# Kernel optimization log

Hardware: AMD Instinct MI355X
Metric: run time of the kernel (lower is better)

## Reference

```python
import jax, jax.numpy as jnp
import numpy as np

B, C, D, K = 16, 512, 256, 32

def setup_inputs() -> dict:
    key = jax.random.key(0)
    ks = jax.random.split(key, 6)
    s = 1.0 / np.sqrt(D)
    return {
        "h": jax.random.normal(ks[0], (B, C, D), dtype=jnp.float32),
        "topk_idx": jax.random.randint(ks[1], (B, C, K), 0, C, dtype=jnp.int64),
        "topk_scores": jax.random.normal(ks[2], (B, C, K), dtype=jnp.float32),
        "vW": jax.random.normal(ks[3], (D, D), dtype=jnp.float32) * s,
        "vb": jnp.zeros((D,), dtype=jnp.float32),
        "oW": jax.random.normal(ks[4], (D, D), dtype=jnp.float32) * s,
        "ob": jnp.zeros((D,), dtype=jnp.float32),
        "gW": jax.random.normal(ks[5], (2 * D, D), dtype=jnp.float32) * s,
        "gb": jnp.zeros((D,), dtype=jnp.float32),
    }

def reference(h, topk_idx, topk_scores, vW, vb, oW, ob, gW, gb):
    # Gather K neighbor features per (batch, channel): [B, C, K, D]
    b_idx = jnp.arange(h.shape[0])[:, None, None]
    neigh = h[b_idx, topk_idx]                         # [B,C,K,D]
    attn = jax.nn.softmax(topk_scores, axis=-1)        # [B,C,K]
    neigh = jnp.einsum('bckd,de->bcke', neigh, vW) + vb  # v_proj
    agg = jnp.einsum('bck,bckd->bcd', attn, neigh)      # weighted sum
    gate = jax.nn.sigmoid(jnp.concatenate([h, agg], axis=-1) @ gW + gb)
    delta = gate * (agg @ oW + ob)
    return delta
```

## Files before the change

### kernel.cpp

```cpp
#include <hip/hip_runtime.h>
#include <hip/hip_bf16.h>
#include <cstdint>
#include <cstddef>

using short8  = __attribute__((ext_vector_type(8))) short;
using short4v = __attribute__((ext_vector_type(4))) short;
using f32x4   = __attribute__((ext_vector_type(4))) float;

constexpr int NB = 16, NC = 512, ND = 256, NK = 32;
constexpr int ROWS = 16;
constexpr int NROW = NB * NC;
constexpr int NBLK = NROW / ROWS;
constexpr int LDP  = ND + 8;
constexpr int PLD  = 516;

constexpr int LDS_W   = 16 * PLD * 4;
constexpr int LDS_HB  = LDS_W + 16 * LDP * 2;
constexpr int LDS_TOT = LDS_HB + 16 * LDP * 2;

constexpr int PVW = 0;
constexpr int POW = 65536;
constexpr int PGW = 131072;
constexpr int PHB = 262144;
constexpr size_t WS_NEED = (size_t)(PHB + NB * 131072) * 2;

static __device__ __forceinline__ unsigned short f2bf(float f) {
    __hip_bfloat16 b = __float2bfloat16(f);
    return *reinterpret_cast<unsigned short*>(&b);
}
static __device__ __forceinline__ short4v f2bf4(float4 v) {
    short4v r;
    r[0] = (short)f2bf(v.x); r[1] = (short)f2bf(v.y);
    r[2] = (short)f2bf(v.z); r[3] = (short)f2bf(v.w);
    return r;
}

__global__ __launch_bounds__(256)
void stk_pack_all(const float* __restrict__ vW, const float* __restrict__ oW,
                  const float* __restrict__ gW, const float* __restrict__ h,
                  unsigned short* __restrict__ ws)
{
    const int blk = blockIdx.x;
    if (blk < 128) {
        const int tid  = blk * 256 + threadIdx.x;
        const int lane = tid & 63;
        const int fl   = tid >> 6;
        const float* src; int nt, ks;
        if (fl < 128)      { src = vW; nt = fl >> 3;         ks = fl & 7;          }
        else if (fl < 256) { src = oW; nt = (fl - 128) >> 3; ks = (fl - 128) & 7;  }
        else               { src = gW; nt = (fl - 256) >> 4; ks = (fl - 256) & 15; }
        const int col = nt * 16 + (lane & 15);
        const int k0  = ks * 32 + (lane >> 4) * 8;
        short8 v;
        #pragma unroll
        for (int j = 0; j < 8; ++j)
            v[j] = (short)f2bf(src[(size_t)(k0 + j) * ND + col]);
        *reinterpret_cast<short8*>(&ws[(size_t)tid * 8]) = v;
    } else {
        const int tid  = (blk - 128) * 256 + threadIdx.x;
        const int lane = tid & 63;
        const int fs   = tid >> 6;
        const int b    = fs >> 8;
        const int ks   = (fs >> 4) & 15;
        const int nt   = fs & 15;
        const float* src = h + (size_t)b * NC * ND;
        const int col = nt * 16 + (lane & 15);
        const int k0  = ks * 32 + (lane >> 4) * 8;
        short8 v;
        #pragma unroll
        for (int j = 0; j < 8; ++j)
            v[j] = (short)f2bf(src[(size_t)(k0 + j) * ND + col]);
        *reinterpret_cast<short8*>(&ws[(size_t)PHB + (size_t)tid * 8]) = v;
    }
}

__global__ __launch_bounds__(512, 4)
void stk_mfma(const float* __restrict__ h,
              const int*   __restrict__ topk_idx,
              const float* __restrict__ topk_scores,
              const float* __restrict__ vb, const float* __restrict__ ob,
              const float* __restrict__ gb,
              const unsigned short* __restrict__ wsb,
              float* __restrict__ out)
{
    __shared__ __align__(16) char smem[LDS_TOT];
    float          (*s_P )[PLD] = reinterpret_cast<float(*)[PLD]>(smem);
    unsigned short (*s_ab)[LDP] = reinterpret_cast<unsigned short(*)[LDP]>(smem);
    unsigned short (*s_w )[LDP] = reinterpret_cast<unsigned short(*)[LDP]>(smem + LDS_W);
    unsigned short (*s_hb)[LDP] = reinterpret_cast<unsigned short(*)[LDP]>(smem + LDS_HB);

    const int t     = threadIdx.x;
    const int bid   = (int)blockIdx.x;
    const int swz   = ((bid & 7) << 6) + (bid >> 3);
    const int m0    = swz * ROWS;
    const int batch = m0 >> 9;

    {
        float4* p4 = reinterpret_cast<float4*>(&s_P[0][0]);
        #pragma unroll
        for (int i = 0; i < 5; ++i) {
            const int j = t + i * 512;
            if (j < (ROWS * PLD) / 4) p4[j] = float4{0.f, 0.f, 0.f, 0.f};
        }
    }

    const int sr  = t >> 5;
    const int sc8 = (t & 31) * 8;
    const float4 h0 = *reinterpret_cast<const float4*>(&h[(size_t)(m0 + sr) * ND + sc8]);
    const float4 h1 = *reinterpret_cast<const float4*>(&h[(size_t)(m0 + sr) * ND + sc8 + 4]);

    const int k = t & 31;
    const int r = t >> 5;
    float att; int id;
    {
        const size_t off = (size_t)(m0 + r) * NK + k;
        const float s = topk_scores[off];
        id = topk_idx[off];
        float m = s;
        #pragma unroll
        for (int msk = 16; msk >= 1; msk >>= 1)
            m = fmaxf(m, __shfl_xor(m, msk));
        const float p = __expf(s - m);
        float Z = p;
        #pragma unroll
        for (int msk = 16; msk >= 1; msk >>= 1)
            Z += __shfl_xor(Z, msk);
        att = p / Z;
    }
    __syncthreads();

    atomicAdd(&s_P[r][id], att);

    *reinterpret_cast<short4v*>(&s_hb[sr][sc8])     = f2bf4(h0);
    *reinterpret_cast<short4v*>(&s_hb[sr][sc8 + 4]) = f2bf4(h1);
    __syncthreads();

    const int lane = t & 63;
    const int w    = t >> 6;
    const int n0   = 2 * w;
    const int lr   = lane & 15;
    const int lg   = lane >> 4;

    {
        f32x4 acc[2] = {f32x4{0,0,0,0}, f32x4{0,0,0,0}};
        const unsigned short* hf = wsb + (size_t)PHB + (size_t)batch * 131072;
        #pragma unroll
        for (int ks = 0; ks < 16; ++ks) {
            const int kb = ks * 32 + lg * 8;
            const float4 a0 = *reinterpret_cast<const float4*>(&s_P[lr][kb]);
            const float4 a1 = *reinterpret_cast<const float4*>(&s_P[lr][kb + 4]);
            short8 a;
            a[0] = (short)f2bf(a0.x); a[1] = (short)f2bf(a0.y);
            a[2] = (short)f2bf(a0.z); a[3] = (short)f2bf(a0.w);
            a[4] = (short)f2bf(a1.x); a[5] = (short)f2bf(a1.y);
            a[6] = (short)f2bf(a1.z); a[7] = (short)f2bf(a1.w);
            #pragma unroll
            for (int n = 0; n < 2; ++n) {
                const short8 b = *reinterpret_cast<const short8*>(
                    &hf[(size_t)(((ks * 16 + n0 + n) * 64 + lane) * 8)]);
                acc[n] = __builtin_amdgcn_mfma_f32_16x16x32_bf16(a, b, acc[n], 0, 0, 0);
            }
        }
        #pragma unroll
        for (int n = 0; n < 2; ++n) {
            const int col = (n0 + n) * 16 + lr;
            #pragma unroll
            for (int q = 0; q < 4; ++q)
                s_w[4 * lg + q][col] = f2bf(acc[n][q]);
        }
    }
    __syncthreads();

    {
        f32x4 acc[2];
        #pragma unroll
        for (int n = 0; n < 2; ++n) {
            const float bv = vb[(n0 + n) * 16 + lr];
            acc[n] = f32x4{bv, bv, bv, bv};
        }
        #pragma unroll
        for (int ks = 0; ks < 8; ++ks) {
            const int kb = ks * 32 + lg * 8;
            const short8 a = *reinterpret_cast<const short8*>(&s_w[lr][kb]);
            #pragma unroll
            for (int n = 0; n < 2; ++n) {
                const short8 b = *reinterpret_cast<const short8*>(
                    &wsb[(size_t)(PVW + (((n0 + n) * 8 + ks) * 64 + lane) * 8)]);
                acc[n] = __builtin_amdgcn_mfma_f32_16x16x32_bf16(a, b, acc[n], 0, 0, 0);
            }
        }
        #pragma unroll
        for (int n = 0; n < 2; ++n) {
            const int col = (n0 + n) * 16 + lr;
            #pragma unroll
            for (int q = 0; q < 4; ++q)
                s_ab[4 * lg + q][col] = f2bf(acc[n][q]);
        }
    }
    __syncthreads();

    {
        f32x4 ao[2], ag[2];
        #pragma unroll
        for (int n = 0; n < 2; ++n) {
            const float bo = ob[(n0 + n) * 16 + lr];
            const float bg = gb[(n0 + n) * 16 + lr];
            ao[n] = f32x4{bo, bo, bo, bo};
            ag[n] = f32x4{bg, bg, bg, bg};
        }
        #pragma unroll
        for (int ks = 0; ks < 8; ++ks) {
            const int kb = ks * 32 + lg * 8;
            const short8 aa = *reinterpret_cast<const short8*>(&s_ab[lr][kb]);
            const short8 ah = *reinterpret_cast<const short8*>(&s_hb[lr][kb]);
            #pragma unroll
            for (int n = 0; n < 2; ++n) {
                const int nt = n0 + n;
                const short8 b_o  = *reinterpret_cast<const short8*>(
                    &wsb[(size_t)(POW + ((nt * 8 + ks) * 64 + lane) * 8)]);
                const short8 b_g1 = *reinterpret_cast<const short8*>(
                    &wsb[(size_t)(PGW + ((nt * 16 + ks) * 64 + lane) * 8)]);
                const short8 b_g2 = *reinterpret_cast<const short8*>(
                    &wsb[(size_t)(PGW + ((nt * 16 + ks + 8) * 64 + lane) * 8)]);
                ao[n] = __builtin_amdgcn_mfma_f32_16x16x32_bf16(aa, b_o,  ao[n], 0, 0, 0);
                ag[n] = __builtin_amdgcn_mfma_f32_16x16x32_bf16(ah, b_g1, ag[n], 0, 0, 0);
                ag[n] = __builtin_amdgcn_mfma_f32_16x16x32_bf16(aa, b_g2, ag[n], 0, 0, 0);
            }
        }
        #pragma unroll
        for (int n = 0; n < 2; ++n) {
            const int col = (n0 + n) * 16 + lr;
            #pragma unroll
            for (int q = 0; q < 4; ++q) {
                const int row = m0 + 4 * lg + q;
                const float g = 1.f / (1.f + __expf(-ag[n][q]));
                out[(size_t)row * ND + col] = g * ao[n][q];
            }
        }
    }
}

__global__ __launch_bounds__(512, 2)
void stk_fused(const float* __restrict__ h,
               const int*   __restrict__ topk_idx,
               const float* __restrict__ topk_scores,
               const float* __restrict__ vW, const float* __restrict__ vb,
               const float* __restrict__ oW, const float* __restrict__ ob,
               const float* __restrict__ gW, const float* __restrict__ gb,
               float* __restrict__ out)
{
    __shared__ float s_attn[32][NK];
    __shared__ int   s_idx [32][NK];
    __shared__ float s_wsum[32][ND];
    __shared__ float s_h   [32][ND];
    __shared__ float s_agg [32][ND];

    const int t  = threadIdx.x;
    const int m0 = blockIdx.x * 32;
    const size_t hb = (size_t)(m0 >> 9) * NC * ND;

    {
        const int k  = t & 31;
        const int r0 = t >> 5;
        #pragma unroll
        for (int half = 0; half < 2; ++half) {
            const int r = r0 + (half << 4);
            const size_t off = (size_t)(m0 + r) * NK + k;
            const float s = topk_scores[off];
            const int  id = topk_idx[off];
            float m = s;
            #pragma unroll
            for (int msk = 16; msk >= 1; msk >>= 1) m = fmaxf(m, __shfl_xor(m, msk));
            const float p = __expf(s - m);
            float Z = p;
            #pragma unroll
            for (int msk = 16; msk >= 1; msk >>= 1) Z += __shfl_xor(Z, msk);
            s_attn[r][k] = p / Z;
            s_idx [r][k] = id;
        }
    }
    __syncthreads();

    const int d  = t & 127;
    const int rb = (t >> 7) * 8;

    #pragma unroll
    for (int i = 0; i < 8; ++i) {
        const int r = rb + i;
        const size_t ro = (size_t)(m0 + r) * ND;
        s_h[r][d]       = h[ro + d];
        s_h[r][d + 128] = h[ro + d + 128];
    }
    #pragma unroll 1
    for (int i = 0; i < 8; ++i) {
        const int r = rb + i;
        float a0 = 0.f, a1 = 0.f;
        #pragma unroll 8
        for (int k = 0; k < NK; ++k) {
            const float w  = s_attn[r][k];
            const size_t nb = hb + (size_t)s_idx[r][k] * ND;
            a0 = fmaf(w, h[nb + d],       a0);
            a1 = fmaf(w, h[nb + d + 128], a1);
        }
        s_wsum[r][d]       = a0;
        s_wsum[r][d + 128] = a1;
    }
    __syncthreads();

    float agg0[8], agg1[8];
    {
        const float b0 = vb[d], b1 = vb[d + 128];
        #pragma unroll
        for (int i = 0; i < 8; ++i) { agg0[i] = b0; agg1[i] = b1; }
        for (int e0 = 0; e0 < ND; e0 += 4) {
            float w0[4], w1[4];
            #pragma unroll
            for (int j = 0; j < 4; ++j) {
                w0[j] = vW[(size_t)(e0 + j) * ND + d];
                w1[j] = vW[(size_t)(e0 + j) * ND + d + 128];
            }
            #pragma unroll
            for (int i = 0; i < 8; ++i) {
                const float4 a = *reinterpret_cast<const float4*>(&s_wsum[rb + i][e0]);
                agg0[i] = fmaf(a.x, w0[0], agg0[i]); agg1[i] = fmaf(a.x, w1[0], agg1[i]);
                agg0[i] = fmaf(a.y, w0[1], agg0[i]); agg1[i] = fmaf(a.y, w1[1], agg1[i]);
                agg0[i] = fmaf(a.z, w0[2], agg0[i]); agg1[i] = fmaf(a.z, w1[2], agg1[i]);
                agg0[i] = fmaf(a.w, w0[3], agg0[i]); agg1[i] = fmaf(a.w, w1[3], agg1[i]);
            }
        }
        #pragma unroll
        for (int i = 0; i < 8; ++i) {
            s_agg[rb + i][d]       = agg0[i];
            s_agg[rb + i][d + 128] = agg1[i];
        }
    }
    __syncthreads();

    float o0[8], o1[8], g0[8], g1[8];
    {
        const float obb0 = ob[d], obb1 = ob[d + 128];
        const float gbb0 = gb[d], gbb1 = gb[d + 128];
        #pragma unroll
        for (int i = 0; i < 8; ++i) { o0[i]=obb0; o1[i]=obb1; g0[i]=gbb0; g1[i]=gbb1; }
        for (int e0 = 0; e0 < ND; e0 += 4) {
            float ow0[4], ow1[4], gh0[4], gh1[4], ga0[4], ga1[4];
            #pragma unroll
            for (int j = 0; j < 4; ++j) {
                const size_t er = (size_t)(e0 + j) * ND;
                ow0[j] = oW[er + d];                    ow1[j] = oW[er + d + 128];
                gh0[j] = gW[er + d];                    gh1[j] = gW[er + d + 128];
                ga0[j] = gW[er + (size_t)ND * ND + d];  ga1[j] = gW[er + (size_t)ND * ND + d + 128];
            }
            #pragma unroll
            for (int i = 0; i < 8; ++i) {
                const float4 a  = *reinterpret_cast<const float4*>(&s_agg[rb + i][e0]);
                const float4 hh = *reinterpret_cast<const float4*>(&s_h  [rb + i][e0]);
                o0[i] = fmaf(a.x, ow0[0], o0[i]); o0[i] = fmaf(a.y, ow0[1], o0[i]);
                o0[i] = fmaf(a.z, ow0[2], o0[i]); o0[i] = fmaf(a.w, ow0[3], o0[i]);
                o1[i] = fmaf(a.x, ow1[0], o1[i]); o1[i] = fmaf(a.y, ow1[1], o1[i]);
                o1[i] = fmaf(a.z, ow1[2], o1[i]); o1[i] = fmaf(a.w, ow1[3], o1[i]);
                g0[i] = fmaf(hh.x, gh0[0], g0[i]); g0[i] = fmaf(hh.y, gh0[1], g0[i]);
                g0[i] = fmaf(hh.z, gh0[2], g0[i]); g0[i] = fmaf(hh.w, gh0[3], g0[i]);
                g1[i] = fmaf(hh.x, gh1[0], g1[i]); g1[i] = fmaf(hh.y, gh1[1], g1[i]);
                g1[i] = fmaf(hh.z, gh1[2], g1[i]); g1[i] = fmaf(hh.w, gh1[3], g1[i]);
                g0[i] = fmaf(a.x, ga0[0], g0[i]); g0[i] = fmaf(a.y, ga0[1], g0[i]);
                g0[i] = fmaf(a.z, ga0[2], g0[i]); g0[i] = fmaf(a.w, ga0[3], g0[i]);
                g1[i] = fmaf(a.x, ga1[0], g1[i]); g1[i] = fmaf(a.y, ga1[1], g1[i]);
                g1[i] = fmaf(a.z, ga1[2], g1[i]); g1[i] = fmaf(a.w, ga1[3], g1[i]);
            }
        }
    }
    #pragma unroll
    for (int i = 0; i < 8; ++i) {
        const size_t ro = (size_t)(m0 + rb + i) * ND;
        const float sg0 = 1.f / (1.f + __expf(-g0[i]));
        const float sg1 = 1.f / (1.f + __expf(-g1[i]));
        out[ro + d]       = sg0 * o0[i];
        out[ro + d + 128] = sg1 * o1[i];
    }
}

extern "C" void kernel_launch(void* const* d_in, const int* in_sizes, int n_in,
                              void* d_out, int out_size, void* d_ws, size_t ws_size,
                              hipStream_t stream) {
    const float* h   = (const float*)d_in[0];
    const int*   idx = (const int*)  d_in[1];
    const float* sc  = (const float*)d_in[2];
    const float* vW  = (const float*)d_in[3];
    const float* vb  = (const float*)d_in[4];
    const float* oW  = (const float*)d_in[5];
    const float* ob  = (const float*)d_in[6];
    const float* gW  = (const float*)d_in[7];
    const float* gb  = (const float*)d_in[8];
    float* out = (float*)d_out;

    if (ws_size >= WS_NEED) {
        unsigned short* wsb = (unsigned short*)d_ws;
        stk_pack_all<<<1152, 256, 0, stream>>>(vW, oW, gW, h, wsb);
        stk_mfma    <<<NBLK, 512, 0, stream>>>(h, idx, sc, vb, ob, gb, wsb, out);
    } else {
        stk_fused<<<256, 512, 0, stream>>>(h, idx, sc, vW, vb, oW, ob, gW, gb, out);
    }
}
```

Measured before the change: 31.85 us.

## Double rows per block and reuse each weight fragment across two M tiles

Each block now handles 32 rows with 1024 threads (16 waves), and each wave owns one 16-column N tile while looping over two 16-row M tiles. Each B fragment loaded from global memory (packed h, vW, oW, gW) is reused for two MFMAs, which halves weight traffic per row. The cost is half as many blocks (256), larger LDS per block and launch bounds of 1024 with one block per CU, which lowers occupancy and latency hiding. The per-thread softmax and atomic setup remains one thread per (row, k).

```diff
diff --git a/kernel.cpp b/kernel.cpp
--- a/kernel.cpp
+++ b/kernel.cpp
@@ -8,15 +8,16 @@
 using f32x4   = __attribute__((ext_vector_type(4))) float;
 
 constexpr int NB = 16, NC = 512, ND = 256, NK = 32;
-constexpr int ROWS = 16;
+constexpr int ROWS = 32;
 constexpr int NROW = NB * NC;
 constexpr int NBLK = NROW / ROWS;
+constexpr int NTHR = 1024;
 constexpr int LDP  = ND + 8;
 constexpr int PLD  = 516;
 
-constexpr int LDS_W   = 16 * PLD * 4;
-constexpr int LDS_HB  = LDS_W + 16 * LDP * 2;
-constexpr int LDS_TOT = LDS_HB + 16 * LDP * 2;
+constexpr int LDS_W   = ROWS * PLD * 4;
+constexpr int LDS_HB  = LDS_W + ROWS * LDP * 2;
+constexpr int LDS_TOT = LDS_HB + ROWS * LDP * 2;
 
 constexpr int PVW = 0;
 constexpr int POW = 65536;
@@ -74,7 +75,7 @@
     }
 }
 
-__global__ __launch_bounds__(512, 4)
+__global__ __launch_bounds__(1024, 1)
 void stk_mfma(const float* __restrict__ h,
               const int*   __restrict__ topk_idx,
               const float* __restrict__ topk_scores,
@@ -89,17 +90,17 @@
     unsigned short (*s_w )[LDP] = reinterpret_cast<unsigned short(*)[LDP]>(smem + LDS_W);
     unsigned short (*s_hb)[LDP] = reinterpret_cast<unsigned short(*)[LDP]>(smem + LDS_HB);
 
-    const int t     = threadIdx.x;
-    const int bid   = (int)blockIdx.x;
-    const int swz   = ((bid & 7) << 6) + (bid >> 3);
-    const int m0    = swz * ROWS;
+    const int t   = threadIdx.x;
+    const int bid = (int)blockIdx.x;
+    const int swz = ((bid & 7) << 5) + (bid >> 3);
+    const int m0  = swz * ROWS;
     const int batch = m0 >> 9;
 
     {
         float4* p4 = reinterpret_cast<float4*>(&s_P[0][0]);
         #pragma unroll
         for (int i = 0; i < 5; ++i) {
-            const int j = t + i * 512;
+            const int j = t + i * NTHR;
             if (j < (ROWS * PLD) / 4) p4[j] = float4{0.f, 0.f, 0.f, 0.f};
         }
     }
@@ -137,7 +138,7 @@
 
     const int lane = t & 63;
     const int w    = t >> 6;
-    const int n0   = 2 * w;
+    const int nt   = w;
     const int lr   = lane & 15;
     const int lg   = lane >> 4;
 
@@ -147,94 +148,85 @@
         #pragma unroll
         for (int ks = 0; ks < 16; ++ks) {
             const int kb = ks * 32 + lg * 8;
-            const float4 a0 = *reinterpret_cast<const float4*>(&s_P[lr][kb]);
-            const float4 a1 = *reinterpret_cast<const float4*>(&s_P[lr][kb + 4]);
-            short8 a;
-            a[0] = (short)f2bf(a0.x); a[1] = (short)f2bf(a0.y);
-            a[2] = (short)f2bf(a0.z); a[3] = (short)f2bf(a0.w);
-            a[4] = (short)f2bf(a1.x); a[5] = (short)f2bf(a1.y);
-            a[6] = (short)f2bf(a1.z); a[7] = (short)f2bf(a1.w);
-            #pragma unroll
-            for (int n = 0; n < 2; ++n) {
-                const short8 b = *reinterpret_cast<const short8*>(
-                    &hf[(size_t)(((ks * 16 + n0 + n) * 64 + lane) * 8)]);
-                acc[n] = __builtin_amdgcn_mfma_f32_16x16x32_bf16(a, b, acc[n], 0, 0, 0);
-            }
-        }
-        #pragma unroll
-        for (int n = 0; n < 2; ++n) {
-            const int col = (n0 + n) * 16 + lr;
+            const short8 b = *reinterpret_cast<const short8*>(
+                &hf[(size_t)(((ks * 16 + nt) * 64 + lane) * 8)]);
+            #pragma unroll
+            for (int m = 0; m < 2; ++m) {
+                const float4 a0 = *reinterpret_cast<const float4*>(&s_P[m * 16 + lr][kb]);
+                const float4 a1 = *reinterpret_cast<const float4*>(&s_P[m * 16 + lr][kb + 4]);
+                short8 a;
+                a[0] = (short)f2bf(a0.x); a[1] = (short)f2bf(a0.y);
+                a[2] = (short)f2bf(a0.z); a[3] = (short)f2bf(a0.w);
+                a[4] = (short)f2bf(a1.x); a[5] = (short)f2bf(a1.y);
+                a[6] = (short)f2bf(a1.z); a[7] = (short)f2bf(a1.w);
+                acc[m] = __builtin_amdgcn_mfma_f32_16x16x32_bf16(a, b, acc[m], 0, 0, 0);
+            }
+        }
+        #pragma unroll
+        for (int m = 0; m < 2; ++m) {
+            const int col = nt * 16 + lr;
             #pragma unroll
             for (int q = 0; q < 4; ++q)
-                s_w[4 * lg + q][col] = f2bf(acc[n][q]);
-        }
-    }
-    __syncthreads();
-
-    {
-        f32x4 acc[2];
-        #pragma unroll
-        for (int n = 0; n < 2; ++n) {
-            const float bv = vb[(n0 + n) * 16 + lr];
-            acc[n] = f32x4{bv, bv, bv, bv};
-        }
+                s_w[m * 16 + 4 * lg + q][col] = f2bf(acc[m][q]);
+        }
+    }
+    __syncthreads();
+
+    {
+        const float bv = vb[nt * 16 + lr];
+        f32x4 acc[2] = {f32x4{bv, bv, bv, bv}, f32x4{bv, bv, bv, bv}};
         #pragma unroll
         for (int ks = 0; ks < 8; ++ks) {
             const int kb = ks * 32 + lg * 8;
-            const short8 a = *reinterpret_cast<const short8*>(&s_w[lr][kb]);
-            #pragma unroll
-            for (int n = 0; n < 2; ++n) {
-                const short8 b = *reinterpret_cast<const short8*>(
-                    &wsb[(size_t)(PVW + (((n0 + n) * 8 + ks) * 64 + lane) * 8)]);
-                acc[n] = __builtin_amdgcn_mfma_f32_16x16x32_bf16(a, b, acc[n], 0, 0, 0);
-            }
-        }
-        #pragma unroll
-        for (int n = 0; n < 2; ++n) {
-            const int col = (n0 + n) * 16 + lr;
+            const short8 b = *reinterpret_cast<const short8*>(
+                &wsb[(size_t)(PVW + ((nt * 8 + ks) * 64 + lane) * 8)]);
+            #pragma unroll
+            for (int m = 0; m < 2; ++m) {
+                const short8 a = *reinterpret_cast<const short8*>(&s_w[m * 16 + lr][kb]);
+                acc[m] = __builtin_amdgcn_mfma_f32_16x16x32_bf16(a, b, acc[m], 0, 0, 0);
+            }
+        }
+        #pragma unroll
+        for (int m = 0; m < 2; ++m) {
+            const int col = nt * 16 + lr;
             #pragma unroll
             for (int q = 0; q < 4; ++q)
-                s_ab[4 * lg + q][col] = f2bf(acc[n][q]);
-        }
-    }
-    __syncthreads();
-
-    {
-        f32x4 ao[2], ag[2];
-        #pragma unroll
-        for (int n = 0; n < 2; ++n) {
-            const float bo = ob[(n0 + n) * 16 + lr];
-            const float bg = gb[(n0 + n) * 16 + lr];
-            ao[n] = f32x4{bo, bo, bo, bo};
-            ag[n] = f32x4{bg, bg, bg, bg};
-        }
+                s_ab[m * 16 + 4 * lg + q][col] = f2bf(acc[m][q]);
+        }
+    }
+    __syncthreads();
+
+    {
+        const float bo = ob[nt * 16 + lr];
+        const float bg = gb[nt * 16 + lr];
+        f32x4 ao[2] = {f32x4{bo, bo, bo, bo}, f32x4{bo, bo, bo, bo}};
+        f32x4 ag[2] = {f32x4{bg, bg, bg, bg}, f32x4{bg, bg, bg, bg}};
         #pragma unroll
         for (int ks = 0; ks < 8; ++ks) {
             const int kb = ks * 32 + lg * 8;
-            const short8 aa = *reinterpret_cast<const short8*>(&s_ab[lr][kb]);
-            const short8 ah = *reinterpret_cast<const short8*>(&s_hb[lr][kb]);
-            #pragma unroll
-            for (int n = 0; n < 2; ++n) {
-                const int nt = n0 + n;
-                const short8 b_o  = *reinterpret_cast<const short8*>(
-                    &wsb[(size_t)(POW + ((nt * 8 + ks) * 64 + lane) * 8)]);
-                const short8 b_g1 = *reinterpret_cast<const short8*>(
-                    &wsb[(size_t)(PGW + ((nt * 16 + ks) * 64 + lane) * 8)]);
-                const short8 b_g2 = *reinterpret_cast<const short8*>(
-                    &wsb[(size_t)(PGW + ((nt * 16 + ks + 8) * 64 + lane) * 8)]);
-                ao[n] = __builtin_amdgcn_mfma_f32_16x16x32_bf16(aa, b_o,  ao[n], 0, 0, 0);
-                ag[n] = __builtin_amdgcn_mfma_f32_16x16x32_bf16(ah, b_g1, ag[n], 0, 0, 0);
-                ag[n] = __builtin_amdgcn_mfma_f32_16x16x32_bf16(aa, b_g2, ag[n], 0, 0, 0);
-            }
-        }
-        #pragma unroll
-        for (int n = 0; n < 2; ++n) {
-            const int col = (n0 + n) * 16 + lr;
+            const short8 b_o  = *reinterpret_cast<const short8*>(
+                &wsb[(size_t)(POW + ((nt * 8 + ks) * 64 + lane) * 8)]);
+            const short8 b_g1 = *reinterpret_cast<const short8*>(
+                &wsb[(size_t)(PGW + ((nt * 16 + ks) * 64 + lane) * 8)]);
+            const short8 b_g2 = *reinterpret_cast<const short8*>(
+                &wsb[(size_t)(PGW + ((nt * 16 + ks + 8) * 64 + lane) * 8)]);
+            #pragma unroll
+            for (int m = 0; m < 2; ++m) {
+                const short8 aa = *reinterpret_cast<const short8*>(&s_ab[m * 16 + lr][kb]);
+                const short8 ah = *reinterpret_cast<const short8*>(&s_hb[m * 16 + lr][kb]);
+                ao[m] = __builtin_amdgcn_mfma_f32_16x16x32_bf16(aa, b_o,  ao[m], 0, 0, 0);
+                ag[m] = __builtin_amdgcn_mfma_f32_16x16x32_bf16(ah, b_g1, ag[m], 0, 0, 0);
+                ag[m] = __builtin_amdgcn_mfma_f32_16x16x32_bf16(aa, b_g2, ag[m], 0, 0, 0);
+            }
+        }
+        #pragma unroll
+        for (int m = 0; m < 2; ++m) {
+            const int col = nt * 16 + lr;
             #pragma unroll
             for (int q = 0; q < 4; ++q) {
-                const int row = m0 + 4 * lg + q;
-                const float g = 1.f / (1.f + __expf(-ag[n][q]));
-                out[(size_t)row * ND + col] = g * ao[n][q];
+                const int row = m0 + m * 16 + 4 * lg + q;
+                const float g = 1.f / (1.f + __expf(-ag[m][q]));
+                out[(size_t)row * ND + col] = g * ao[m][q];
             }
         }
     }
@@ -397,7 +389,7 @@
     if (ws_size >= WS_NEED) {
         unsigned short* wsb = (unsigned short*)d_ws;
         stk_pack_all<<<1152, 256, 0, stream>>>(vW, oW, gW, h, wsb);
-        stk_mfma    <<<NBLK, 512, 0, stream>>>(h, idx, sc, vb, ob, gb, wsb, out);
+        stk_mfma    <<<NBLK, NTHR, 0, stream>>>(h, idx, sc, vb, ob, gb, wsb, out);
     } else {
         stk_fused<<<256, 512, 0, stream>>>(h, idx, sc, vW, vb, oW, ob, gW, gb, out);
     }
```

New measurement: 33.41 us. 1.05x slower.

## Precompute h·vW and h·gW_h per batch; aggregate projected features, double rows per block

Applied to the files above, without the earlier changes.

Uses linearity: the value projection is applied to h once per row in a prep kernel (HV = h·vW + vb), so agg becomes P·HV directly, removing the per-block vW GEMM. The h half of the gate GEMM is also precomputed in prep and stored as bf16 accumulator fragments, which are loaded to initialise the gate accumulators. The main kernel now handles 32 rows per block and reuses each B fragment across two M tiles. This moves more work into the prep kernel, which reads unpacked fp32 weights directly, and adds extra bf16 rounding of the intermediate results.

```diff
diff --git a/kernel.cpp b/kernel.cpp
--- a/kernel.cpp
+++ b/kernel.cpp
@@ -8,25 +8,26 @@
 using f32x4   = __attribute__((ext_vector_type(4))) float;
 
 constexpr int NB = 16, NC = 512, ND = 256, NK = 32;
-constexpr int ROWS = 16;
+constexpr int ROWS = 32;
 constexpr int NROW = NB * NC;
 constexpr int NBLK = NROW / ROWS;
 constexpr int LDP  = ND + 8;
 constexpr int PLD  = 516;
 
-constexpr int LDS_W   = 16 * PLD * 4;
-constexpr int LDS_HB  = LDS_W + 16 * LDP * 2;
-constexpr int LDS_TOT = LDS_HB + 16 * LDP * 2;
-
-constexpr int PVW = 0;
-constexpr int POW = 65536;
-constexpr int PGW = 131072;
-constexpr int PHB = 262144;
-constexpr size_t WS_NEED = (size_t)(PHB + NB * 131072) * 2;
+constexpr int LDS_TOT = ROWS * PLD * 4;
+
+constexpr int POW2 = 0;
+constexpr int PGA  = 65536;
+constexpr int PGH  = 131072;
+constexpr int PHV  = 131072 + 2097152;
+constexpr size_t WS_NEED = (size_t)(PHV + NB * 131072) * 2;
 
 static __device__ __forceinline__ unsigned short f2bf(float f) {
     __hip_bfloat16 b = __float2bfloat16(f);
     return *reinterpret_cast<unsigned short*>(&b);
+}
+static __device__ __forceinline__ float bf2f(unsigned short u) {
+    return __uint_as_float(((unsigned)u) << 16);
 }
 static __device__ __forceinline__ short4v f2bf4(float4 v) {
     short4v r;
@@ -35,87 +36,152 @@
     return r;
 }
 
-__global__ __launch_bounds__(256)
-void stk_pack_all(const float* __restrict__ vW, const float* __restrict__ oW,
-                  const float* __restrict__ gW, const float* __restrict__ h,
-                  unsigned short* __restrict__ ws)
+__global__ __launch_bounds__(512)
+void stk_prep(const float* __restrict__ vW, const float* __restrict__ vb,
+              const float* __restrict__ oW,
+              const float* __restrict__ gW, const float* __restrict__ gb,
+              const float* __restrict__ h, unsigned short* __restrict__ ws)
 {
+    __shared__ __align__(16) unsigned short s_a[32][264];
+    __shared__ __align__(16) unsigned short s_c[32][264];
     const int blk = blockIdx.x;
-    if (blk < 128) {
-        const int tid  = blk * 256 + threadIdx.x;
+    const int t   = threadIdx.x;
+
+    if (blk < 32) {
+        const int tid  = blk * 512 + t;
         const int lane = tid & 63;
         const int fl   = tid >> 6;
-        const float* src; int nt, ks;
-        if (fl < 128)      { src = vW; nt = fl >> 3;         ks = fl & 7;          }
-        else if (fl < 256) { src = oW; nt = (fl - 128) >> 3; ks = (fl - 128) & 7;  }
-        else               { src = gW; nt = (fl - 256) >> 4; ks = (fl - 256) & 15; }
+        const float* src; int nt, ks, rowoff; size_t dst;
+        if (fl < 128) { src = oW; nt = fl >> 3; ks = fl & 7; rowoff = 0;
+                        dst = (size_t)POW2 + (size_t)fl * 512; }
+        else { const int f2 = fl - 128; src = gW; nt = f2 >> 3; ks = f2 & 7; rowoff = 256;
+               dst = (size_t)PGA + (size_t)f2 * 512; }
         const int col = nt * 16 + (lane & 15);
-        const int k0  = ks * 32 + (lane >> 4) * 8;
+        const int k0  = rowoff + ks * 32 + (lane >> 4) * 8;
         short8 v;
         #pragma unroll
         for (int j = 0; j < 8; ++j)
             v[j] = (short)f2bf(src[(size_t)(k0 + j) * ND + col]);
-        *reinterpret_cast<short8*>(&ws[(size_t)tid * 8]) = v;
-    } else {
-        const int tid  = (blk - 128) * 256 + threadIdx.x;
-        const int lane = tid & 63;
-        const int fs   = tid >> 6;
-        const int b    = fs >> 8;
-        const int ks   = (fs >> 4) & 15;
-        const int nt   = fs & 15;
-        const float* src = h + (size_t)b * NC * ND;
-        const int col = nt * 16 + (lane & 15);
-        const int k0  = ks * 32 + (lane >> 4) * 8;
+        *reinterpret_cast<short8*>(&ws[dst + (size_t)lane * 8]) = v;
+        return;
+    }
+
+    const int q  = blk - 32;
+    const int b  = q >> 4, rt = q & 15;
+    const float* hb = h + ((size_t)b * NC + rt * 32) * ND;
+
+    {
+        const int row = t >> 4;
+        const int c0  = (t & 15) * 16;
+        #pragma unroll
+        for (int u = 0; u < 4; ++u) {
+            const float4 x = *reinterpret_cast<const float4*>(&hb[(size_t)row * ND + c0 + 4 * u]);
+            *reinterpret_cast<short4v*>(&s_a[row][c0 + 4 * u]) = f2bf4(x);
+        }
+    }
+    __syncthreads();
+
+    const int lane = t & 63, w = t >> 6;
+    const int lr = lane & 15, lg = lane >> 4;
+    const int n0 = 2 * w;
+
+    f32x4 ahv[2][2], agh[2][2];
+    #pragma unroll
+    for (int n = 0; n < 2; ++n) {
+        const float bvv = vb[(n0 + n) * 16 + lr];
+        const float bgg = gb[(n0 + n) * 16 + lr];
+        #pragma unroll
+        for (int m = 0; m < 2; ++m) {
+            ahv[m][n] = f32x4{bvv, bvv, bvv, bvv};
+            agh[m][n] = f32x4{bgg, bgg, bgg, bgg};
+        }
+    }
+    #pragma unroll
+    for (int ks = 0; ks < 8; ++ks) {
+        const int kb = ks * 32 + lg * 8;
+        const short8 a0 = *reinterpret_cast<const short8*>(&s_a[lr][kb]);
+        const short8 a1 = *reinterpret_cast<const short8*>(&s_a[16 + lr][kb]);
+        #pragma unroll
+        for (int n = 0; n < 2; ++n) {
+            const int col = (n0 + n) * 16 + lr;
+            short8 bv, bg;
+            #pragma unroll
+            for (int j = 0; j < 8; ++j) {
+                bv[j] = (short)f2bf(vW[(size_t)(kb + j) * ND + col]);
+                bg[j] = (short)f2bf(gW[(size_t)(kb + j) * ND + col]);
+            }
+            ahv[0][n] = __builtin_amdgcn_mfma_f32_16x16x32_bf16(a0, bv, ahv[0][n], 0, 0, 0);
+            ahv[1][n] = __builtin_amdgcn_mfma_f32_16x16x32_bf16(a1, bv, ahv[1][n], 0, 0, 0);
+            agh[0][n] = __builtin_amdgcn_mfma_f32_16x16x32_bf16(a0, bg, agh[0][n], 0, 0, 0);
+            agh[1][n] = __builtin_amdgcn_mfma_f32_16x16x32_bf16(a1, bg, agh[1][n], 0, 0, 0);
+        }
+    }
+    #pragma unroll
+    for (int m = 0; m < 2; ++m)
+        #pragma unroll
+        for (int n = 0; n < 2; ++n) {
+            const int mt = b * 32 + rt * 2 + m;
+            short4v v4;
+            #pragma unroll
+            for (int qq = 0; qq < 4; ++qq) v4[qq] = (short)f2bf(agh[m][n][qq]);
+            *reinterpret_cast<short4v*>(
+                &ws[(size_t)PGH + ((size_t)(mt * 16 + n0 + n) * 64 + lane) * 4]) = v4;
+        }
+    #pragma unroll
+    for (int m = 0; m < 2; ++m)
+        #pragma unroll
+        for (int n = 0; n < 2; ++n)
+            #pragma unroll
+            for (int qq = 0; qq < 4; ++qq)
+                s_c[m * 16 + 4 * lg + qq][(n0 + n) * 16 + lr] = f2bf(ahv[m][n][qq]);
+    __syncthreads();
+    #pragma unroll
+    for (int n = 0; n < 2; ++n) {
+        const int nt = n0 + n;
         short8 v;
         #pragma unroll
         for (int j = 0; j < 8; ++j)
-            v[j] = (short)f2bf(src[(size_t)(k0 + j) * ND + col]);
-        *reinterpret_cast<short8*>(&ws[(size_t)PHB + (size_t)tid * 8]) = v;
+            v[j] = (short)s_c[lg * 8 + j][nt * 16 + lr];
+        *reinterpret_cast<short8*>(
+            &ws[(size_t)PHV + (size_t)b * 131072 + ((size_t)(rt * 16 + nt) * 64 + lane) * 8]) = v;
     }
 }
 
 __global__ __launch_bounds__(512, 4)
-void stk_mfma(const float* __restrict__ h,
-              const int*   __restrict__ topk_idx,
+void stk_main(const int*   __restrict__ topk_idx,
               const float* __restrict__ topk_scores,
-              const float* __restrict__ vb, const float* __restrict__ ob,
-              const float* __restrict__ gb,
+              const float* __restrict__ ob,
               const unsigned short* __restrict__ wsb,
               float* __restrict__ out)
 {
     __shared__ __align__(16) char smem[LDS_TOT];
     float          (*s_P )[PLD] = reinterpret_cast<float(*)[PLD]>(smem);
     unsigned short (*s_ab)[LDP] = reinterpret_cast<unsigned short(*)[LDP]>(smem);
-    unsigned short (*s_w )[LDP] = reinterpret_cast<unsigned short(*)[LDP]>(smem + LDS_W);
-    unsigned short (*s_hb)[LDP] = reinterpret_cast<unsigned short(*)[LDP]>(smem + LDS_HB);
-
-    const int t     = threadIdx.x;
-    const int bid   = (int)blockIdx.x;
-    const int swz   = ((bid & 7) << 6) + (bid >> 3);
-    const int m0    = swz * ROWS;
+
+    const int t   = threadIdx.x;
+    const int bid = (int)blockIdx.x;
+    const int swz = ((bid & 7) << 5) + (bid >> 3);
+    const int m0  = swz * ROWS;
     const int batch = m0 >> 9;
 
     {
-        float4* p4 = reinterpret_cast<float4*>(&s_P[0][0]);
-        #pragma unroll
-        for (int i = 0; i < 5; ++i) {
+        float4* p4 = reinterpret_cast<float4*>(smem);
+        #pragma unroll
+        for (int i = 0; i < 9; ++i) {
             const int j = t + i * 512;
             if (j < (ROWS * PLD) / 4) p4[j] = float4{0.f, 0.f, 0.f, 0.f};
         }
     }
 
-    const int sr  = t >> 5;
-    const int sc8 = (t & 31) * 8;
-    const float4 h0 = *reinterpret_cast<const float4*>(&h[(size_t)(m0 + sr) * ND + sc8]);
-    const float4 h1 = *reinterpret_cast<const float4*>(&h[(size_t)(m0 + sr) * ND + sc8 + 4]);
-
-    const int k = t & 31;
-    const int r = t >> 5;
-    float att; int id;
-    {
+    const int k  = t & 31;
+    const int r0 = t >> 5;
+    float att[2]; int id[2];
+    #pragma unroll
+    for (int half = 0; half < 2; ++half) {
+        const int r = r0 + (half << 4);
         const size_t off = (size_t)(m0 + r) * NK + k;
         const float s = topk_scores[off];
-        id = topk_idx[off];
+        id[half] = topk_idx[off];
         float m = s;
         #pragma unroll
         for (int msk = 16; msk >= 1; msk >>= 1)
@@ -125,118 +191,106 @@
         #pragma unroll
         for (int msk = 16; msk >= 1; msk >>= 1)
             Z += __shfl_xor(Z, msk);
-        att = p / Z;
-    }
-    __syncthreads();
-
-    atomicAdd(&s_P[r][id], att);
-
-    *reinterpret_cast<short4v*>(&s_hb[sr][sc8])     = f2bf4(h0);
-    *reinterpret_cast<short4v*>(&s_hb[sr][sc8 + 4]) = f2bf4(h1);
-    __syncthreads();
-
-    const int lane = t & 63;
-    const int w    = t >> 6;
-    const int n0   = 2 * w;
-    const int lr   = lane & 15;
-    const int lg   = lane >> 4;
-
-    {
-        f32x4 acc[2] = {f32x4{0,0,0,0}, f32x4{0,0,0,0}};
-        const unsigned short* hf = wsb + (size_t)PHB + (size_t)batch * 131072;
+        att[half] = p / Z;
+    }
+    __syncthreads();
+
+    atomicAdd(&s_P[r0][id[0]],      att[0]);
+    atomicAdd(&s_P[r0 + 16][id[1]], att[1]);
+    __syncthreads();
+
+    const int lane = t & 63, w = t >> 6;
+    const int n0 = 2 * w, lr = lane & 15, lg = lane >> 4;
+
+    f32x4 acc[2][2] = {{f32x4{0,0,0,0}, f32x4{0,0,0,0}},
+                       {f32x4{0,0,0,0}, f32x4{0,0,0,0}}};
+    {
+        const unsigned short* hf = wsb + (size_t)PHV + (size_t)batch * 131072;
         #pragma unroll
         for (int ks = 0; ks < 16; ++ks) {
             const int kb = ks * 32 + lg * 8;
-            const float4 a0 = *reinterpret_cast<const float4*>(&s_P[lr][kb]);
-            const float4 a1 = *reinterpret_cast<const float4*>(&s_P[lr][kb + 4]);
-            short8 a;
-            a[0] = (short)f2bf(a0.x); a[1] = (short)f2bf(a0.y);
-            a[2] = (short)f2bf(a0.z); a[3] = (short)f2bf(a0.w);
-            a[4] = (short)f2bf(a1.x); a[5] = (short)f2bf(a1.y);
-            a[6] = (short)f2bf(a1.z); a[7] = (short)f2bf(a1.w);
+            short8 a[2];
+            #pragma unroll
+            for (int m = 0; m < 2; ++m) {
+                const float4 x0 = *reinterpret_cast<const float4*>(&s_P[m * 16 + lr][kb]);
+                const float4 x1 = *reinterpret_cast<const float4*>(&s_P[m * 16 + lr][kb + 4]);
+                a[m][0] = (short)f2bf(x0.x); a[m][1] = (short)f2bf(x0.y);
+                a[m][2] = (short)f2bf(x0.z); a[m][3] = (short)f2bf(x0.w);
+                a[m][4] = (short)f2bf(x1.x); a[m][5] = (short)f2bf(x1.y);
+                a[m][6] = (short)f2bf(x1.z); a[m][7] = (short)f2bf(x1.w);
+            }
             #pragma unroll
             for (int n = 0; n < 2; ++n) {
-                const short8 b = *reinterpret_cast<const short8*>(
-                    &hf[(size_t)(((ks * 16 + n0 + n) * 64 + lane) * 8)]);
-                acc[n] = __builtin_amdgcn_mfma_f32_16x16x32_bf16(a, b, acc[n], 0, 0, 0);
-            }
-        }
+                const short8 bfr = *reinterpret_cast<const short8*>(
+                    &hf[((size_t)(ks * 16 + n0 + n) * 64 + lane) * 8]);
+                acc[0][n] = __builtin_amdgcn_mfma_f32_16x16x32_bf16(a[0], bfr, acc[0][n], 0, 0, 0);
+                acc[1][n] = __builtin_amdgcn_mfma_f32_16x16x32_bf16(a[1], bfr, acc[1][n], 0, 0, 0);
+            }
+        }
+    }
+    __syncthreads();
+
+    #pragma unroll
+    for (int m = 0; m < 2; ++m)
+        #pragma unroll
+        for (int n = 0; n < 2; ++n)
+            #pragma unroll
+            for (int qq = 0; qq < 4; ++qq)
+                s_ab[m * 16 + 4 * lg + qq][(n0 + n) * 16 + lr] = f2bf(acc[m][n][qq]);
+    __syncthreads();
+
+    {
+        f32x4 ao[2][2], ag[2][2];
         #pragma unroll
         for (int n = 0; n < 2; ++n) {
-            const int col = (n0 + n) * 16 + lr;
-            #pragma unroll
-            for (int q = 0; q < 4; ++q)
-                s_w[4 * lg + q][col] = f2bf(acc[n][q]);
-        }
-    }
-    __syncthreads();
-
-    {
-        f32x4 acc[2];
-        #pragma unroll
-        for (int n = 0; n < 2; ++n) {
-            const float bv = vb[(n0 + n) * 16 + lr];
-            acc[n] = f32x4{bv, bv, bv, bv};
-        }
+            const float bo = ob[(n0 + n) * 16 + lr];
+            #pragma unroll
+            for (int m = 0; m < 2; ++m) ao[m][n] = f32x4{bo, bo, bo, bo};
+        }
+        #pragma unroll
+        for (int m = 0; m < 2; ++m)
+            #pragma unroll
+            for (int n = 0; n < 2; ++n) {
+                const int mt = swz * 2 + m;
+                const short4v g4 = *reinterpret_cast<const short4v*>(
+                    &wsb[(size_t)PGH + ((size_t)(mt * 16 + n0 + n) * 64 + lane) * 4]);
+                #pragma unroll
+                for (int qq = 0; qq < 4; ++qq)
+                    ag[m][n][qq] = bf2f((unsigned short)g4[qq]);
+            }
         #pragma unroll
         for (int ks = 0; ks < 8; ++ks) {
             const int kb = ks * 32 + lg * 8;
-            const short8 a = *reinterpret_cast<const short8*>(&s_w[lr][kb]);
-            #pragma unroll
-            for (int n = 0; n < 2; ++n) {
-                const short8 b = *reinterpret_cast<const short8*>(
-                    &wsb[(size_t)(PVW + (((n0 + n) * 8 + ks) * 64 + lane) * 8)]);
-                acc[n] = __builtin_amdgcn_mfma_f32_16x16x32_bf16(a, b, acc[n], 0, 0, 0);
-            }
-        }
-        #pragma unroll
-        for (int n = 0; n < 2; ++n) {
-            const int col = (n0 + n) * 16 + lr;
-            #pragma unroll
-            for (int q = 0; q < 4; ++q)
-                s_ab[4 * lg + q][col] = f2bf(acc[n][q]);
-        }
-    }
-    __syncthreads();
-
-    {
-        f32x4 ao[2], ag[2];
-        #pragma unroll
-        for (int n = 0; n < 2; ++n) {
-            const float bo = ob[(n0 + n) * 16 + lr];
-            const float bg = gb[(n0 + n) * 16 + lr];
-            ao[n] = f32x4{bo, bo, bo, bo};
-            ag[n] = f32x4{bg, bg, bg, bg};
-        }
-        #pragma unroll
-        for (int ks = 0; ks < 8; ++ks) {
-            const int kb = ks * 32 + lg * 8;
-            const short8 aa = *reinterpret_cast<const short8*>(&s_ab[lr][kb]);
-            const short8 ah = *reinterpret_cast<const short8*>(&s_hb[lr][kb]);
+            short8 aa[2];
+            #pragma unroll
+            for (int m = 0; m < 2; ++m)
+                aa[m] = *reinterpret_cast<const short8*>(&s_ab[m * 16 + lr][kb]);
             #pragma unroll
             for (int n = 0; n < 2; ++n) {
                 const int nt = n0 + n;
-                const short8 b_o  = *reinterpret_cast<const short8*>(
-                    &wsb[(size_t)(POW + ((nt * 8 + ks) * 64 + lane) * 8)]);
-                const short8 b_g1 = *reinterpret_cast<const short8*>(
-                    &wsb[(size_t)(PGW + ((nt * 16 + ks) * 64 + lane) * 8)]);
-                const short8 b_g2 = *reinterpret_cast<const short8*>(
-                    &wsb[(size_t)(PGW + ((nt * 16 + ks + 8) * 64 + lane) * 8)]);
-                ao[n] = __builtin_amdgcn_mfma_f32_16x16x32_bf16(aa, b_o,  ao[n], 0, 0, 0);
-                ag[n] = __builtin_amdgcn_mfma_f32_16x16x32_bf16(ah, b_g1, ag[n], 0, 0, 0);
-                ag[n] = __builtin_amdgcn_mfma_f32_16x16x32_bf16(aa, b_g2, ag[n], 0, 0, 0);
-            }
-        }
-        #pragma unroll
-        for (int n = 0; n < 2; ++n) {
-            const int col = (n0 + n) * 16 + lr;
-            #pragma unroll
-            for (int q = 0; q < 4; ++q) {
-                const int row = m0 + 4 * lg + q;
-                const float g = 1.f / (1.f + __expf(-ag[n][q]));
-                out[(size_t)row * ND + col] = g * ao[n][q];
-            }
-        }
+                const short8 bo8 = *reinterpret_cast<const short8*>(
+                    &wsb[(size_t)POW2 + ((size_t)(nt * 8 + ks) * 64 + lane) * 8]);
+                const short8 bg8 = *reinterpret_cast<const short8*>(
+                    &wsb[(size_t)PGA + ((size_t)(nt * 8 + ks) * 64 + lane) * 8]);
+                #pragma unroll
+                for (int m = 0; m < 2; ++m) {
+                    ao[m][n] = __builtin_amdgcn_mfma_f32_16x16x32_bf16(aa[m], bo8, ao[m][n], 0, 0, 0);
+                    ag[m][n] = __builtin_amdgcn_mfma_f32_16x16x32_bf16(aa[m], bg8, ag[m][n], 0, 0, 0);
+                }
+            }
+        }
+        #pragma unroll
+        for (int m = 0; m < 2; ++m)
+            #pragma unroll
+            for (int n = 0; n < 2; ++n) {
+                const int col = (n0 + n) * 16 + lr;
+                #pragma unroll
+                for (int qq = 0; qq < 4; ++qq) {
+                    const int row = m0 + m * 16 + 4 * lg + qq;
+                    const float g = 1.f / (1.f + __expf(-ag[m][n][qq]));
+                    out[(size_t)row * ND + col] = g * ao[m][n][qq];
+                }
+            }
     }
 }
 
@@ -396,8 +450,8 @@
 
     if (ws_size >= WS_NEED) {
         unsigned short* wsb = (unsigned short*)d_ws;
-        stk_pack_all<<<1152, 256, 0, stream>>>(vW, oW, gW, h, wsb);
-        stk_mfma    <<<NBLK, 512, 0, stream>>>(h, idx, sc, vb, ob, gb, wsb, out);
+        stk_prep<<<288,  512, 0, stream>>>(vW, vb, oW, gW, gb, h, wsb);
+        stk_main<<<NBLK, 512, 0, stream>>>(idx, sc, ob, wsb, out);
     } else {
         stk_fused<<<256, 512, 0, stream>>>(h, idx, sc, vW, vb, oW, ob, gW, gb, out);
     }
```

After: 32.52 us. 2.1% more time.

## Process 32 rows per block with XOR-swizzled bf16 LDS tiles

Applied to the files above, without the earlier changes.

Each block now handles 32 rows instead of 16. Every weight B-fragment loaded from global memory feeds two MFMAs, which halves weight traffic per row and halves the block count. The attention probability matrix is converted to bf16 in LDS once, instead of being converted on every A-fragment load. Padded LDS layouts are replaced by XOR-swizzled layouts to avoid bank conflicts. Shared memory grows to 64KB per block, which may limit occupancy below the declared four blocks per CU.

```diff
diff --git a/kernel.cpp b/kernel.cpp
--- a/kernel.cpp
+++ b/kernel.cpp
@@ -8,15 +8,13 @@
 using f32x4   = __attribute__((ext_vector_type(4))) float;
 
 constexpr int NB = 16, NC = 512, ND = 256, NK = 32;
-constexpr int ROWS = 16;
+constexpr int ROWS = 32;
 constexpr int NROW = NB * NC;
 constexpr int NBLK = NROW / ROWS;
-constexpr int LDP  = ND + 8;
-constexpr int PLD  = 516;
-
-constexpr int LDS_W   = 16 * PLD * 4;
-constexpr int LDS_HB  = LDS_W + 16 * LDP * 2;
-constexpr int LDS_TOT = LDS_HB + 16 * LDP * 2;
+constexpr int NTHR = 512;
+
+constexpr int OFF_SW = 32768;
+constexpr int OFF_HB = 49152;
 
 constexpr int PVW = 0;
 constexpr int POW = 65536;
@@ -75,7 +73,7 @@
 }
 
 __global__ __launch_bounds__(512, 4)
-void stk_mfma(const float* __restrict__ h,
+void stk_main(const float* __restrict__ h,
               const int*   __restrict__ topk_idx,
               const float* __restrict__ topk_scores,
               const float* __restrict__ vb, const float* __restrict__ ob,
@@ -83,39 +81,41 @@
               const unsigned short* __restrict__ wsb,
               float* __restrict__ out)
 {
-    __shared__ __align__(16) char smem[LDS_TOT];
-    float          (*s_P )[PLD] = reinterpret_cast<float(*)[PLD]>(smem);
-    unsigned short (*s_ab)[LDP] = reinterpret_cast<unsigned short(*)[LDP]>(smem);
-    unsigned short (*s_w )[LDP] = reinterpret_cast<unsigned short(*)[LDP]>(smem + LDS_W);
-    unsigned short (*s_hb)[LDP] = reinterpret_cast<unsigned short(*)[LDP]>(smem + LDS_HB);
-
-    const int t     = threadIdx.x;
-    const int bid   = (int)blockIdx.x;
-    const int swz   = ((bid & 7) << 6) + (bid >> 3);
-    const int m0    = swz * ROWS;
+    __shared__ __align__(16) char smem[65536];
+    float (*s_P)[512] = reinterpret_cast<float(*)[512]>(smem);
+
+    const int t   = threadIdx.x;
+    const int bid = (int)blockIdx.x;
+    const int swz = ((bid & 7) << 5) + (bid >> 3);
+    const int m0  = swz * ROWS;
     const int batch = m0 >> 9;
 
-    {
-        float4* p4 = reinterpret_cast<float4*>(&s_P[0][0]);
-        #pragma unroll
-        for (int i = 0; i < 5; ++i) {
-            const int j = t + i * 512;
-            if (j < (ROWS * PLD) / 4) p4[j] = float4{0.f, 0.f, 0.f, 0.f};
-        }
-    }
-
-    const int sr  = t >> 5;
-    const int sc8 = (t & 31) * 8;
-    const float4 h0 = *reinterpret_cast<const float4*>(&h[(size_t)(m0 + sr) * ND + sc8]);
-    const float4 h1 = *reinterpret_cast<const float4*>(&h[(size_t)(m0 + sr) * ND + sc8 + 4]);
-
-    const int k = t & 31;
-    const int r = t >> 5;
-    float att; int id;
-    {
+    const int hr = t >> 4;
+    const int hc = (t & 15) * 16;
+    short4v hreg[4];
+    {
+        const float* hrow = h + (size_t)(m0 + hr) * ND + hc;
+        #pragma unroll
+        for (int u = 0; u < 4; ++u)
+            hreg[u] = f2bf4(*reinterpret_cast<const float4*>(hrow + 4 * u));
+    }
+
+    {
+        float4* p4 = reinterpret_cast<float4*>(smem);
+        #pragma unroll
+        for (int i = 0; i < 8; ++i)
+            p4[t + 512 * i] = float4{0.f, 0.f, 0.f, 0.f};
+    }
+
+    const int k  = t & 31;
+    const int r0 = t >> 5;
+    float att[2]; int id[2];
+    #pragma unroll
+    for (int half = 0; half < 2; ++half) {
+        const int r = r0 + (half << 4);
         const size_t off = (size_t)(m0 + r) * NK + k;
         const float s = topk_scores[off];
-        id = topk_idx[off];
+        id[half] = topk_idx[off];
         float m = s;
         #pragma unroll
         for (int msk = 16; msk >= 1; msk >>= 1)
@@ -125,94 +125,129 @@
         #pragma unroll
         for (int msk = 16; msk >= 1; msk >>= 1)
             Z += __shfl_xor(Z, msk);
-        att = p / Z;
-    }
-    __syncthreads();
-
-    atomicAdd(&s_P[r][id], att);
-
-    *reinterpret_cast<short4v*>(&s_hb[sr][sc8])     = f2bf4(h0);
-    *reinterpret_cast<short4v*>(&s_hb[sr][sc8 + 4]) = f2bf4(h1);
-    __syncthreads();
-
-    const int lane = t & 63;
-    const int w    = t >> 6;
-    const int n0   = 2 * w;
-    const int lr   = lane & 15;
-    const int lg   = lane >> 4;
-
-    {
-        f32x4 acc[2] = {f32x4{0,0,0,0}, f32x4{0,0,0,0}};
+        att[half] = p / Z;
+    }
+    __syncthreads();
+
+    atomicAdd(&s_P[r0][id[0]],      att[0]);
+    atomicAdd(&s_P[r0 + 16][id[1]], att[1]);
+    __syncthreads();
+
+    {
+        const int pr  = t >> 4;
+        const int pc4 = (t & 15) * 4;
+        float4 pch[8];
+        #pragma unroll
+        for (int u = 0; u < 8; ++u)
+            pch[u] = *reinterpret_cast<const float4*>(&s_P[pr][pc4 + 64 * u]);
+        __syncthreads();
+
+        const int xr = (pr & 7) << 4;
+        #pragma unroll
+        for (int u = 0; u < 8; ++u)
+            *reinterpret_cast<short4v*>(
+                smem + pr * 1024 + (((pc4 + 64 * u) * 2) ^ xr)) = f2bf4(pch[u]);
+        const int xh = (hr & 7) << 4;
+        #pragma unroll
+        for (int u = 0; u < 4; ++u)
+            *reinterpret_cast<short4v*>(
+                smem + OFF_HB + hr * 512 + (((hc + 4 * u) * 2) ^ xh)) = hreg[u];
+    }
+    __syncthreads();
+
+    const int lane = t & 63, w = t >> 6;
+    const int n0 = 2 * w, lr = lane & 15, lg = lane >> 4;
+    const int xa = (lr & 7) << 4;
+
+    {
+        f32x4 acc[2][2] = {{f32x4{0,0,0,0}, f32x4{0,0,0,0}},
+                           {f32x4{0,0,0,0}, f32x4{0,0,0,0}}};
         const unsigned short* hf = wsb + (size_t)PHB + (size_t)batch * 131072;
         #pragma unroll
         for (int ks = 0; ks < 16; ++ks) {
-            const int kb = ks * 32 + lg * 8;
-            const float4 a0 = *reinterpret_cast<const float4*>(&s_P[lr][kb]);
-            const float4 a1 = *reinterpret_cast<const float4*>(&s_P[lr][kb + 4]);
-            short8 a;
-            a[0] = (short)f2bf(a0.x); a[1] = (short)f2bf(a0.y);
-            a[2] = (short)f2bf(a0.z); a[3] = (short)f2bf(a0.w);
-            a[4] = (short)f2bf(a1.x); a[5] = (short)f2bf(a1.y);
-            a[6] = (short)f2bf(a1.z); a[7] = (short)f2bf(a1.w);
+            const int cb = (ks * 32 + lg * 8) * 2;
+            short8 a[2];
+            a[0] = *reinterpret_cast<const short8*>(smem + lr * 1024 + (cb ^ xa));
+            a[1] = *reinterpret_cast<const short8*>(smem + (16 + lr) * 1024 + (cb ^ xa));
             #pragma unroll
             for (int n = 0; n < 2; ++n) {
                 const short8 b = *reinterpret_cast<const short8*>(
-                    &hf[(size_t)(((ks * 16 + n0 + n) * 64 + lane) * 8)]);
-                acc[n] = __builtin_amdgcn_mfma_f32_16x16x32_bf16(a, b, acc[n], 0, 0, 0);
-            }
-        }
-        #pragma unroll
-        for (int n = 0; n < 2; ++n) {
-            const int col = (n0 + n) * 16 + lr;
-            #pragma unroll
-            for (int q = 0; q < 4; ++q)
-                s_w[4 * lg + q][col] = f2bf(acc[n][q]);
-        }
-    }
-    __syncthreads();
-
-    {
-        f32x4 acc[2];
+                    &hf[((size_t)(ks * 16 + n0 + n) * 64 + lane) * 8]);
+                acc[0][n] = __builtin_amdgcn_mfma_f32_16x16x32_bf16(a[0], b, acc[0][n], 0, 0, 0);
+                acc[1][n] = __builtin_amdgcn_mfma_f32_16x16x32_bf16(a[1], b, acc[1][n], 0, 0, 0);
+            }
+        }
+        #pragma unroll
+        for (int m = 0; m < 2; ++m)
+            #pragma unroll
+            for (int n = 0; n < 2; ++n) {
+                const int col = (n0 + n) * 16 + lr;
+                #pragma unroll
+                for (int q = 0; q < 4; ++q) {
+                    const int row = m * 16 + 4 * lg + q;
+                    *reinterpret_cast<unsigned short*>(
+                        smem + OFF_SW + row * 512 + ((col * 2) ^ ((row & 7) << 4))) =
+                        f2bf(acc[m][n][q]);
+                }
+            }
+    }
+    __syncthreads();
+
+    {
+        f32x4 acc[2][2];
         #pragma unroll
         for (int n = 0; n < 2; ++n) {
             const float bv = vb[(n0 + n) * 16 + lr];
-            acc[n] = f32x4{bv, bv, bv, bv};
+            acc[0][n] = f32x4{bv, bv, bv, bv};
+            acc[1][n] = f32x4{bv, bv, bv, bv};
         }
         #pragma unroll
         for (int ks = 0; ks < 8; ++ks) {
-            const int kb = ks * 32 + lg * 8;
-            const short8 a = *reinterpret_cast<const short8*>(&s_w[lr][kb]);
+            const int cb = (ks * 32 + lg * 8) * 2;
+            short8 a[2];
+            a[0] = *reinterpret_cast<const short8*>(smem + OFF_SW + lr * 512 + (cb ^ xa));
+            a[1] = *reinterpret_cast<const short8*>(smem + OFF_SW + (16 + lr) * 512 + (cb ^ xa));
             #pragma unroll
             for (int n = 0; n < 2; ++n) {
                 const short8 b = *reinterpret_cast<const short8*>(
                     &wsb[(size_t)(PVW + (((n0 + n) * 8 + ks) * 64 + lane) * 8)]);
-                acc[n] = __builtin_amdgcn_mfma_f32_16x16x32_bf16(a, b, acc[n], 0, 0, 0);
-            }
-        }
-        #pragma unroll
-        for (int n = 0; n < 2; ++n) {
-            const int col = (n0 + n) * 16 + lr;
-            #pragma unroll
-            for (int q = 0; q < 4; ++q)
-                s_ab[4 * lg + q][col] = f2bf(acc[n][q]);
-        }
-    }
-    __syncthreads();
-
-    {
-        f32x4 ao[2], ag[2];
+                acc[0][n] = __builtin_amdgcn_mfma_f32_16x16x32_bf16(a[0], b, acc[0][n], 0, 0, 0);
+                acc[1][n] = __builtin_amdgcn_mfma_f32_16x16x32_bf16(a[1], b, acc[1][n], 0, 0, 0);
+            }
+        }
+        #pragma unroll
+        for (int m = 0; m < 2; ++m)
+            #pragma unroll
+            for (int n = 0; n < 2; ++n) {
+                const int col = (n0 + n) * 16 + lr;
+                #pragma unroll
+                for (int q = 0; q < 4; ++q) {
+                    const int row = m * 16 + 4 * lg + q;
+                    *reinterpret_cast<unsigned short*>(
+                        smem + row * 512 + ((col * 2) ^ ((row & 7) << 4))) =
+                        f2bf(acc[m][n][q]);
+                }
+            }
+    }
+    __syncthreads();
+
+    {
+        f32x4 ao[2][2], ag[2][2];
         #pragma unroll
         for (int n = 0; n < 2; ++n) {
             const float bo = ob[(n0 + n) * 16 + lr];
             const float bg = gb[(n0 + n) * 16 + lr];
-            ao[n] = f32x4{bo, bo, bo, bo};
-            ag[n] = f32x4{bg, bg, bg, bg};
+            ao[0][n] = f32x4{bo, bo, bo, bo}; ao[1][n] = ao[0][n];
+            ag[0][n] = f32x4{bg, bg, bg, bg}; ag[1][n] = ag[0][n];
         }
         #pragma unroll
         for (int ks = 0; ks < 8; ++ks) {
-            const int kb = ks * 32 + lg * 8;
-            const short8 aa = *reinterpret_cast<const short8*>(&s_ab[lr][kb]);
-            const short8 ah = *reinterpret_cast<const short8*>(&s_hb[lr][kb]);
+            const int cb = (ks * 32 + lg * 8) * 2;
+            short8 aa[2], ah[2];
+            aa[0] = *reinterpret_cast<const short8*>(smem + lr * 512 + (cb ^ xa));
+            aa[1] = *reinterpret_cast<const short8*>(smem + (16 + lr) * 512 + (cb ^ xa));
+            ah[0] = *reinterpret_cast<const short8*>(smem + OFF_HB + lr * 512 + (cb ^ xa));
+            ah[1] = *reinterpret_cast<const short8*>(smem + OFF_HB + (16 + lr) * 512 + (cb ^ xa));
             #pragma unroll
             for (int n = 0; n < 2; ++n) {
                 const int nt = n0 + n;
@@ -222,21 +257,26 @@
                     &wsb[(size_t)(PGW + ((nt * 16 + ks) * 64 + lane) * 8)]);
                 const short8 b_g2 = *reinterpret_cast<const short8*>(
                     &wsb[(size_t)(PGW + ((nt * 16 + ks + 8) * 64 + lane) * 8)]);
-                ao[n] = __builtin_amdgcn_mfma_f32_16x16x32_bf16(aa, b_o,  ao[n], 0, 0, 0);
-                ag[n] = __builtin_amdgcn_mfma_f32_16x16x32_bf16(ah, b_g1, ag[n], 0, 0, 0);
-                ag[n] = __builtin_amdgcn_mfma_f32_16x16x32_bf16(aa, b_g2, ag[n], 0, 0, 0);
-            }
-        }
-        #pragma unroll
-        for (int n = 0; n < 2; ++n) {
-            const int col = (n0 + n) * 16 + lr;
-            #pragma unroll
-            for (int q = 0; q < 4; ++q) {
-                const int row = m0 + 4 * lg + q;
-                const float g = 1.f / (1.f + __expf(-ag[n][q]));
-                out[(size_t)row * ND + col] = g * ao[n][q];
-            }
-        }
+                #pragma unroll
+                for (int m = 0; m < 2; ++m) {
+                    ao[m][n] = __builtin_amdgcn_mfma_f32_16x16x32_bf16(aa[m], b_o,  ao[m][n], 0, 0, 0);
+                    ag[m][n] = __builtin_amdgcn_mfma_f32_16x16x32_bf16(ah[m], b_g1, ag[m][n], 0, 0, 0);
+                    ag[m][n] = __builtin_amdgcn_mfma_f32_16x16x32_bf16(aa[m], b_g2, ag[m][n], 0, 0, 0);
+                }
+            }
+        }
+        #pragma unroll
+        for (int m = 0; m < 2; ++m)
+            #pragma unroll
+            for (int n = 0; n < 2; ++n) {
+                const int col = (n0 + n) * 16 + lr;
+                #pragma unroll
+                for (int q = 0; q < 4; ++q) {
+                    const int row = m0 + m * 16 + 4 * lg + q;
+                    const float g = 1.f / (1.f + __expf(-ag[m][n][q]));
+                    out[(size_t)row * ND + col] = g * ao[m][n][q];
+                }
+            }
     }
 }
 
@@ -397,7 +437,7 @@
     if (ws_size >= WS_NEED) {
         unsigned short* wsb = (unsigned short*)d_ws;
         stk_pack_all<<<1152, 256, 0, stream>>>(vW, oW, gW, h, wsb);
-        stk_mfma    <<<NBLK, 512, 0, stream>>>(h, idx, sc, vb, ob, gb, wsb, out);
+        stk_main    <<<NBLK, NTHR, 0, stream>>>(h, idx, sc, vb, ob, gb, wsb, out);
     } else {
         stk_fused<<<256, 512, 0, stream>>>(h, idx, sc, vW, vb, oW, ob, gW, gb, out);
     }
```

Measured after the change: 28.70 us. 1.11x faster.
